# Kernel tuning notes

Measured on AMD Instinct MI355X. Metric: run time of the kernel, lower is better.

## Reference

```python
import jax, jax.numpy as jnp
import numpy as np

N = 50000
E = 800000
NEG_SLOPE = 0.2


def gatv2_layer(x, src, dst, Wl, Wr, att, bias, heads, ch):
    # x: [N, Fin]; Wl/Wr: [Fin, heads*ch]; att: [heads, ch]; bias: [heads*ch]
    xl = (x @ Wl).reshape(N, heads, ch)  # source transform
    xr = (x @ Wr).reshape(N, heads, ch)  # target transform
    e = xl[src] + xr[dst]                              # [E, H, C]
    s = jnp.einsum('ehc,hc->eh', jax.nn.leaky_relu(e, NEG_SLOPE), att)  # [E, H]
    # scatter-softmax over incoming edges of each target node
    smax = jax.ops.segment_max(s, dst, num_segments=N)  # [N, H]
    ex = jnp.exp(s - smax[dst])
    denom = jax.ops.segment_sum(ex, dst, num_segments=N)
    alpha = ex / denom[dst]                             # [E, H]
    out = jax.ops.segment_sum(xl[src] * alpha[..., None], dst, num_segments=N)  # [N, H, C]
    return out.reshape(N, heads * ch) + bias


def setup_inputs() -> dict:
    key = jax.random.key(0)
    ks = jax.random.split(key, 12)
    x = jax.random.normal(ks[0], (N, 128), dtype=jnp.float32)
    edge_index = jax.random.randint(ks[1], (2, E), 0, N, dtype=jnp.int64)
    edge_attr = jax.random.normal(ks[2], (E, 16), dtype=jnp.float32)
    s1 = 1.0 / np.sqrt(128.0)
    # layer 1: 128 -> 64, heads=2 (concat -> 128)
    Wl1 = jax.random.normal(ks[3], (128, 128), dtype=jnp.float32) * s1
    Wr1 = jax.random.normal(ks[4], (128, 128), dtype=jnp.float32) * s1
    att1 = jax.random.normal(ks[5], (2, 64), dtype=jnp.float32) * 0.1
    b1 = jnp.zeros((128,), dtype=jnp.float32)
    # layer 2: 128 -> 128, heads=1
    Wl2 = jax.random.normal(ks[6], (128, 128), dtype=jnp.float32) * s1
    Wr2 = jax.random.normal(ks[7], (128, 128), dtype=jnp.float32) * s1
    att2 = jax.random.normal(ks[8], (1, 128), dtype=jnp.float32) * 0.1
    b2 = jnp.zeros((128,), dtype=jnp.float32)
    return {"x": x, "edge_index": edge_index, "edge_attr": edge_attr,
            "Wl1": Wl1, "Wr1": Wr1, "att1": att1, "b1": b1,
            "Wl2": Wl2, "Wr2": Wr2, "att2": att2, "b2": b2}


def reference(x, edge_index, edge_attr, Wl1, Wr1, att1, b1, Wl2, Wr2, att2, b2):
    # using_edge_attr=False default path: edge_attr ignored.
    # GATv2Conv default add_self_loops=True
    loops = jnp.arange(N, dtype=edge_index.dtype)
    src = jnp.concatenate([edge_index[0], loops])
    dst = jnp.concatenate([edge_index[1], loops])
    h = gatv2_layer(x, src, dst, Wl1, Wr1, att1, b1, heads=2, ch=64)
    out = gatv2_layer(h, src, dst, Wl2, Wr2, att2, b2, heads=1, ch=128)
    return out
```

## Files before the change

kernel.cpp:

```cpp
#include <hip/hip_runtime.h>

#define NEG_SLOPE 0.2f
#define NPB 256
#define CHUNK 4096
#define BCAP 5120

typedef _Float16 f16x8 __attribute__((ext_vector_type(8)));
typedef _Float16 f16x4 __attribute__((ext_vector_type(4)));
typedef _Float16 f16x2 __attribute__((ext_vector_type(2)));
typedef float    f32x4 __attribute__((ext_vector_type(4)));
typedef float    f32x8 __attribute__((ext_vector_type(8)));

#if defined(__has_builtin)
#if __has_builtin(__builtin_amdgcn_fdot2)
#define HAVE_FDOT2 1
#endif
#endif

__device__ __forceinline__ f32x8 cvt8(f16x8 v) {
    return __builtin_convertvector(v, f32x8);
}

template <int CTRL>
__device__ __forceinline__ float dpp_add(float v) {
    int o = __builtin_amdgcn_update_dpp(0, __builtin_bit_cast(int, v),
                                        CTRL, 0xF, 0xF, true);
    return v + __builtin_bit_cast(float, o);
}

__global__ __launch_bounds__(256) void prep_kernel(
    const float* __restrict__ W0, const float* __restrict__ W1,
    const float* __restrict__ W2, const float* __restrict__ W3,
    _Float16* __restrict__ wt,
    const float* __restrict__ x, _Float16* __restrict__ xh,
    _Float16* __restrict__ xlo, int total, int* __restrict__ gcursor)
{
    int t = threadIdx.x;
    if (blockIdx.x < 256) {
        if (blockIdx.x == 0) gcursor[t] = t * BCAP;
        int idx = blockIdx.x * 256 + t;
        int m = idx >> 14;
        int k = (idx >> 7) & 127;
        int n = idx & 127;
        const float* W = (m == 0) ? W0 : (m == 1) ? W1 : (m == 2) ? W2 : W3;
        wt[m * 16384 + n * 128 + k] = (_Float16)W[k * 128 + n];
    } else {
        int i = (blockIdx.x - 256) * 256 + t;
        if (i * 2 < total) {
            float2 f = *(const float2*)(x + (size_t)i * 2);
            _Float16 h0 = (_Float16)f.x, h1 = (_Float16)f.y;
            _Float16 l0 = (_Float16)(f.x - (float)h0), l1 = (_Float16)(f.y - (float)h1);
            *(f16x2*)(xh  + (size_t)i * 2) = (f16x2){h0, h1};
            *(f16x2*)(xlo + (size_t)i * 2) = (f16x2){l0, l1};
        }
    }
}

__global__ __launch_bounds__(256) void gemm_f16_kernel(
    const _Float16* __restrict__ Ahi, const _Float16* __restrict__ Alo,
    const _Float16* __restrict__ Wt0, const _Float16* __restrict__ Wt1,
    _Float16* __restrict__ Cl, _Float16* __restrict__ Cr, int N)
{
    __shared__ _Float16 ldsW[128 * 136];

    const int tid = threadIdx.x;
    const int wave = tid >> 6;
    const int lane = tid & 63;
    const int mrow = lane & 15;
    const int quad = lane >> 4;
    const int rbase = blockIdx.x * 128 + wave * 32;
    const int sn = tid >> 1, shf = tid & 1;

    float4 stg[8];
    {
        const float4* gp = (const float4*)(Wt0 + sn * 128 + shf * 64);
#pragma unroll
        for (int j = 0; j < 8; j++) stg[j] = gp[j];
    }

    f16x8 ah[2][4], al[2][4];
#pragma unroll
    for (int rt = 0; rt < 2; rt++) {
        int r = rbase + rt * 16 + mrow;
        if (r > N - 1) r = N - 1;
        const _Float16* pa = Ahi + (size_t)r * 128 + quad * 8;
        const _Float16* pl = Alo + (size_t)r * 128 + quad * 8;
#pragma unroll
        for (int s = 0; s < 4; s++) {
            ah[rt][s] = *(const f16x8*)(pa + s * 32);
            al[rt][s] = *(const f16x8*)(pl + s * 32);
        }
    }

    {
        float4* d = (float4*)&ldsW[sn * 136 + shf * 64];
#pragma unroll
        for (int j = 0; j < 8; j++) d[j] = stg[j];
    }
    __syncthreads();

    float4 stg1[8];
    {
        const float4* gp = (const float4*)(Wt1 + sn * 128 + shf * 64);
#pragma unroll
        for (int j = 0; j < 8; j++) stg1[j] = gp[j];
    }

    auto compute_store = [&](_Float16* __restrict__ C) {
        f32x4 acc[2][8];
#pragma unroll
        for (int rt = 0; rt < 2; rt++)
#pragma unroll
            for (int c = 0; c < 8; c++) acc[rt][c] = (f32x4){0.f, 0.f, 0.f, 0.f};

#pragma unroll
        for (int s = 0; s < 4; s++) {
#pragma unroll
            for (int c = 0; c < 8; c++) {
                f16x8 bw = *(const f16x8*)&ldsW[(c * 16 + mrow) * 136 + s * 32 + quad * 8];
                acc[0][c] = __builtin_amdgcn_mfma_f32_16x16x32_f16(ah[0][s], bw, acc[0][c], 0, 0, 0);
                acc[0][c] = __builtin_amdgcn_mfma_f32_16x16x32_f16(al[0][s], bw, acc[0][c], 0, 0, 0);
                acc[1][c] = __builtin_amdgcn_mfma_f32_16x16x32_f16(ah[1][s], bw, acc[1][c], 0, 0, 0);
                acc[1][c] = __builtin_amdgcn_mfma_f32_16x16x32_f16(al[1][s], bw, acc[1][c], 0, 0, 0);
            }
        }

#pragma unroll
        for (int rt = 0; rt < 2; rt++)
#pragma unroll
            for (int i = 0; i < 4; i++) {
                int r = rbase + rt * 16 + quad * 4 + i;
                if (r < N) {
                    _Float16* cr = C + (size_t)r * 128 + mrow;
#pragma unroll
                    for (int c = 0; c < 8; c++) cr[c * 16] = (_Float16)acc[rt][c][i];
                }
            }
    };

    compute_store(Cl);

    __syncthreads();
    {
        float4* d = (float4*)&ldsW[sn * 136 + shf * 64];
#pragma unroll
        for (int j = 0; j < 8; j++) d[j] = stg1[j];
    }
    __syncthreads();

    compute_store(Cr);
}

__global__ __launch_bounds__(256) void bucketA_kernel(
    const int* __restrict__ ei, int* __restrict__ gcursor,
    int2* __restrict__ staging, int E)
{
    __shared__ int bh[256];
    __shared__ int bbase[256];
    int t = threadIdx.x;
    bh[t] = 0;
    __syncthreads();
    int base = blockIdx.x * CHUNK;
    int srcv[16], dstv[16], rb[16];
#pragma unroll
    for (int j = 0; j < 16; j++) {
        int e = base + t + j * 256;
        if (e < E) {
            int d = ei[E + e];
            srcv[j] = ei[e];
            dstv[j] = d;
            int bk = d >> 8;
            int r = atomicAdd(&bh[bk], 1);
            rb[j] = (r << 8) | bk;
        } else rb[j] = -1;
    }
    __syncthreads();
    if (bh[t]) bbase[t] = atomicAdd(&gcursor[t], bh[t]);
    __syncthreads();
#pragma unroll
    for (int j = 0; j < 16; j++) {
        if (rb[j] >= 0) {
            int bk = rb[j] & 255, r = rb[j] >> 8;
            staging[bbase[bk] + r] = make_int2(srcv[j], dstv[j]);
        }
    }
}

__global__ __launch_bounds__(256) void passB_kernel(
    const int2* __restrict__ staging, const int* __restrict__ gcursor,
    int* __restrict__ start, int* __restrict__ deg,
    int* __restrict__ sorted_src, int N)
{
    __shared__ int lhist[256], lscan[256], lcur[256];
    int b = blockIdx.x, t = threadIdx.x;
    int r0 = b * BCAP;
    int r1 = gcursor[b];
    lhist[t] = 0;
    __syncthreads();
    for (int i = r0 + t; i < r1; i += 256) atomicAdd(&lhist[staging[i].y & 255], 1);
    __syncthreads();
    int v = lhist[t];
    lscan[t] = v;
    __syncthreads();
    for (int off = 1; off < 256; off <<= 1) {
        int u = (t >= off) ? lscan[t - off] : 0;
        __syncthreads();
        lscan[t] += u;
        __syncthreads();
    }
    int excl = lscan[t] - v;
    int node = b * NPB + t;
    if (node < N) { start[node] = r0 + excl; deg[node] = v; }
    lcur[t] = excl;
    __syncthreads();
    for (int i = r0 + t; i < r1; i += 256) {
        int2 p = staging[i];
        int rank = atomicAdd(&lcur[p.y & 255], 1);
        sorted_src[r0 + rank] = p.x;
    }
}

template <int H, bool BFOUT>
__global__ __launch_bounds__(256) void gat_fused_kernel(
    const _Float16* __restrict__ xl, const _Float16* __restrict__ xr,
    const float* __restrict__ att, const float* __restrict__ bias,
    const int* __restrict__ start, const int* __restrict__ deg,
    const int* __restrict__ sorted_src,
    float* __restrict__ outf, _Float16* __restrict__ oh,
    _Float16* __restrict__ ol, int N)
{
    int node = blockIdx.x * 4 + (threadIdx.x >> 6);
    if (node >= N) return;
    const int lane = threadIdx.x & 63;
    const int g  = lane >> 4;
    const int hl = lane & 15;
    const _Float16 NS = (_Float16)NEG_SLOPE;
    const float L2E = 1.44269504f;

    const f16x8 b4 = *(const f16x8*)(xr + (size_t)node * 128 + hl * 8);
    float4 at0 = *(const float4*)(att + hl * 8);
    float4 at1 = *(const float4*)(att + hl * 8 + 4);
#if defined(HAVE_FDOT2)
    f16x2 av0 = {(_Float16)(at0.x * L2E), (_Float16)(at0.y * L2E)};
    f16x2 av1 = {(_Float16)(at0.z * L2E), (_Float16)(at0.w * L2E)};
    f16x2 av2 = {(_Float16)(at1.x * L2E), (_Float16)(at1.y * L2E)};
    f16x2 av3 = {(_Float16)(at1.z * L2E), (_Float16)(at1.w * L2E)};
#else
    f32x8 avf = {at0.x * L2E, at0.y * L2E, at0.z * L2E, at0.w * L2E,
                 at1.x * L2E, at1.y * L2E, at1.z * L2E, at1.w * L2E};
#endif

    auto score = [&](f16x8 a_) -> float {
        f16x8 t = a_ + b4;
        f16x8 u = __builtin_elementwise_max(t, t * NS);
#if defined(HAVE_FDOT2)
        f16x2 u0 = __builtin_shufflevector(u, u, 0, 1);
        f16x2 u1 = __builtin_shufflevector(u, u, 2, 3);
        f16x2 u2 = __builtin_shufflevector(u, u, 4, 5);
        f16x2 u3 = __builtin_shufflevector(u, u, 6, 7);
        return __builtin_amdgcn_fdot2(u0, av0,
               __builtin_amdgcn_fdot2(u1, av1,
               __builtin_amdgcn_fdot2(u2, av2,
               __builtin_amdgcn_fdot2(u3, av3, 0.f, false), false), false), false);
#else
        f32x8 uf = cvt8(u);
        float p = 0.f;
#pragma unroll
        for (int i = 0; i < 8; i++) p += uf[i] * avf[i];
        return p;
#endif
    };

    auto red = [&](float p) -> float {
        p = dpp_add<0xB1>(p);
        p = dpp_add<0x4E>(p);
        p = dpp_add<0x141>(p);
        if (H == 1) p = dpp_add<0x140>(p);
        return p;
    };

    f32x8 acc = {0.f, 0.f, 0.f, 0.f, 0.f, 0.f, 0.f, 0.f};
    float den = 0.f;

    const int s0 = start[node];
    const int M  = deg[node] + 1;
    const int Kfull = M >> 2;
    const int K     = (M + 3) >> 2;

#define GBODY(B) {                                                          \
        int srcv[B]; f16x8 a[B]; float p[B];                                \
        _Pragma("unroll")                                                   \
        for (int j = 0; j < B; j++) {                                       \
            int iv = 4 * (k + j) + g;                                       \
            int ld = sorted_src[s0 + ((iv > 0) ? iv - 1 : 0)];              \
            srcv[j] = (iv == 0) ? node : ld;                                \
        }                                                                   \
        _Pragma("unroll")                                                   \
        for (int j = 0; j < B; j++)                                         \
            a[j] = *(const f16x8*)(xl + (size_t)srcv[j] * 128 + hl * 8);    \
        _Pragma("unroll")                                                   \
        for (int j = 0; j < B; j++) p[j] = score(a[j]);                     \
        _Pragma("unroll")                                                   \
        for (int j = 0; j < B; j++) p[j] = red(p[j]);                       \
        _Pragma("unroll")                                                   \
        for (int j = 0; j < B; j++) {                                       \
            float e = exp2f(p[j]);                                          \
            den += e;                                                       \
            acc = acc + cvt8(a[j]) * e;                                     \
        }                                                                   \
    }

    int k = 0;
    for (; k + 4 <= Kfull; k += 4) GBODY(4)
    if (k + 2 <= Kfull) { GBODY(2) k += 2; }
    if (k < Kfull)      { GBODY(1) k += 1; }
    if (k < K) {
        int iv = 4 * k + g;
        bool valid = iv < M;
        int ld = sorted_src[s0 + ((iv > 0) ? iv - 1 : 0)];
        int src = (iv == 0) ? node : (valid ? ld : node);
        f16x8 a = *(const f16x8*)(xl + (size_t)src * 128 + hl * 8);
        float p = red(score(a));
        float e = valid ? exp2f(p) : 0.f;
        den += e;
        acc = acc + cvt8(a) * e;
    }
#undef GBODY

    den += __shfl_xor(den, 16, 64);
    den += __shfl_xor(den, 32, 64);
#pragma unroll
    for (int i = 0; i < 8; i++) {
        acc[i] += __shfl_xor(acc[i], 16, 64);
        acc[i] += __shfl_xor(acc[i], 32, 64);
    }

    float inv = 1.0f / den;
    float4 bi0 = *(const float4*)(bias + hl * 8);
    float4 bi1 = *(const float4*)(bias + hl * 8 + 4);
    float o[8];
    o[0] = acc[0] * inv + bi0.x;  o[1] = acc[1] * inv + bi0.y;
    o[2] = acc[2] * inv + bi0.z;  o[3] = acc[3] * inv + bi0.w;
    o[4] = acc[4] * inv + bi1.x;  o[5] = acc[5] * inv + bi1.y;
    o[6] = acc[6] * inv + bi1.z;  o[7] = acc[7] * inv + bi1.w;

    if (lane < 16) {
        if (BFOUT) {
            f16x8 hv, lv;
#pragma unroll
            for (int i = 0; i < 8; i++) {
                _Float16 h = (_Float16)o[i];
                hv[i] = h;
                lv[i] = (_Float16)(o[i] - (float)h);
            }
            *(f16x8*)(oh + (size_t)node * 128 + hl * 8) = hv;
            *(f16x8*)(ol + (size_t)node * 128 + hl * 8) = lv;
        } else {
            *(float4*)(outf + (size_t)node * 128 + hl * 8) =
                make_float4(o[0], o[1], o[2], o[3]);
            *(float4*)(outf + (size_t)node * 128 + hl * 8 + 4) =
                make_float4(o[4], o[5], o[6], o[7]);
        }
    }
}

extern "C" void kernel_launch(void* const* d_in, const int* in_sizes, int n_in,
                              void* d_out, int out_size, void* d_ws, size_t ws_size,
                              hipStream_t stream)
{
    const float* x    = (const float*)d_in[0];
    const int*   ei   = (const int*)d_in[1];
    const float* Wl1  = (const float*)d_in[3];
    const float* Wr1  = (const float*)d_in[4];
    const float* att1 = (const float*)d_in[5];
    const float* b1   = (const float*)d_in[6];
    const float* Wl2  = (const float*)d_in[7];
    const float* Wr2  = (const float*)d_in[8];
    const float* att2 = (const float*)d_in[9];
    const float* b2   = (const float*)d_in[10];
    float* out = (float*)d_out;

    const int N  = in_sizes[0] / 128;
    const int E  = in_sizes[1] / 2;
    const int NB = (N + NPB - 1) / NPB;

    const size_t nf = (size_t)N * 128;
    _Float16* xlf  = (_Float16*)d_ws;
    _Float16* xrf  = xlf + nf;
    _Float16* ah   = xrf + nf;
    _Float16* al   = ah + nf;
    _Float16* wt   = al + nf;
    int* gcursor   = (int*)(wt + 4 * 16384);
    int* start     = gcursor + 256;
    int* deg       = start + N;
    size_t stgoff  = ((size_t)(deg + N) + 7) & ~(size_t)7;
    int2* staging  = (int2*)stgoff;
    int* sorted_src = (int*)(staging + (size_t)NB * BCAP);

    const int grid_chunk = (E + CHUNK - 1) / CHUNK;
    const int node_grid  = (N + 3) / 4;
    const int gemm_gx    = (N + 127) / 128;
    const int split_grid = (int)((nf / 2 + 255) / 256);

    prep_kernel<<<256 + split_grid, 256, 0, stream>>>(
        Wl1, Wr1, Wl2, Wr2, wt, x, ah, al, (int)nf, gcursor);

    bucketA_kernel<<<grid_chunk, 256, 0, stream>>>(ei, gcursor, staging, E);
    passB_kernel<<<NB, 256, 0, stream>>>(staging, gcursor, start, deg,
                                         sorted_src, N);

    gemm_f16_kernel<<<gemm_gx, 256, 0, stream>>>(
        ah, al, wt + 0 * 16384, wt + 1 * 16384, xlf, xrf, N);
    gat_fused_kernel<2, true><<<node_grid, 256, 0, stream>>>(
        xlf, xrf, att1, b1, start, deg, sorted_src, nullptr, ah, al, N);

    gemm_f16_kernel<<<gemm_gx, 256, 0, stream>>>(
        ah, al, wt + 2 * 16384, wt + 3 * 16384, xlf, xrf, N);
    gat_fused_kernel<1, false><<<node_grid, 256, 0, stream>>>(
        xlf, xrf, att2, b2, start, deg, sorted_src, out, nullptr, nullptr, N);
}
```

Measured before the change: 286.5 us.

## Split GEMM over grid y and process two nodes per wave with software-pipelined gathers

The GEMM kernel now handles one weight matrix per block, using blockIdx.y to choose between Wl and Wr. This doubles the grid and drops the second LDS reload and its barriers. The aggregation kernel now has each wave process two target nodes at once and prefetches the next pair of gather groups while scoring the current ones. The aim is more memory-level parallelism to hide gather latency. In exchange, the A rows are loaded twice in the GEMM, and wave work is padded to the larger degree of the two nodes, so some iterations are wasted.

```diff
diff --git a/kernel.cpp b/kernel.cpp
--- a/kernel.cpp
+++ b/kernel.cpp
@@ -61,6 +61,9 @@
     const _Float16* __restrict__ Wt0, const _Float16* __restrict__ Wt1,
     _Float16* __restrict__ Cl, _Float16* __restrict__ Cr, int N)
 {
+    const _Float16* Wt = blockIdx.y ? Wt1 : Wt0;
+    _Float16* C = blockIdx.y ? Cr : Cl;
+
     __shared__ _Float16 ldsW[128 * 136];
 
     const int tid = threadIdx.x;
@@ -69,13 +72,13 @@
     const int mrow = lane & 15;
     const int quad = lane >> 4;
     const int rbase = blockIdx.x * 128 + wave * 32;
+
     const int sn = tid >> 1, shf = tid & 1;
-
     float4 stg[8];
     {
-        const float4* gp = (const float4*)(Wt0 + sn * 128 + shf * 64);
-#pragma unroll
-        for (int j = 0; j < 8; j++) stg[j] = gp[j];
+        const float4* g = (const float4*)(Wt + sn * 128 + shf * 64);
+#pragma unroll
+        for (int j = 0; j < 8; j++) stg[j] = g[j];
     }
 
     f16x8 ah[2][4], al[2][4];
@@ -97,58 +100,38 @@
 #pragma unroll
         for (int j = 0; j < 8; j++) d[j] = stg[j];
     }
-    __syncthreads();
-
-    float4 stg1[8];
-    {
-        const float4* gp = (const float4*)(Wt1 + sn * 128 + shf * 64);
-#pragma unroll
-        for (int j = 0; j < 8; j++) stg1[j] = gp[j];
-    }
-
-    auto compute_store = [&](_Float16* __restrict__ C) {
-        f32x4 acc[2][8];
-#pragma unroll
-        for (int rt = 0; rt < 2; rt++)
-#pragma unroll
-            for (int c = 0; c < 8; c++) acc[rt][c] = (f32x4){0.f, 0.f, 0.f, 0.f};
-
-#pragma unroll
-        for (int s = 0; s < 4; s++) {
-#pragma unroll
-            for (int c = 0; c < 8; c++) {
-                f16x8 bw = *(const f16x8*)&ldsW[(c * 16 + mrow) * 136 + s * 32 + quad * 8];
-                acc[0][c] = __builtin_amdgcn_mfma_f32_16x16x32_f16(ah[0][s], bw, acc[0][c], 0, 0, 0);
-                acc[0][c] = __builtin_amdgcn_mfma_f32_16x16x32_f16(al[0][s], bw, acc[0][c], 0, 0, 0);
-                acc[1][c] = __builtin_amdgcn_mfma_f32_16x16x32_f16(ah[1][s], bw, acc[1][c], 0, 0, 0);
-                acc[1][c] = __builtin_amdgcn_mfma_f32_16x16x32_f16(al[1][s], bw, acc[1][c], 0, 0, 0);
+
+    f32x4 acc[2][8];
+#pragma unroll
+    for (int rt = 0; rt < 2; rt++)
+#pragma unroll
+        for (int c = 0; c < 8; c++) acc[rt][c] = (f32x4){0.f, 0.f, 0.f, 0.f};
+
+    __syncthreads();
+
+#pragma unroll
+    for (int s = 0; s < 4; s++) {
+#pragma unroll
+        for (int c = 0; c < 8; c++) {
+            f16x8 bw = *(const f16x8*)&ldsW[(c * 16 + mrow) * 136 + s * 32 + quad * 8];
+            acc[0][c] = __builtin_amdgcn_mfma_f32_16x16x32_f16(ah[0][s], bw, acc[0][c], 0, 0, 0);
+            acc[0][c] = __builtin_amdgcn_mfma_f32_16x16x32_f16(al[0][s], bw, acc[0][c], 0, 0, 0);
+            acc[1][c] = __builtin_amdgcn_mfma_f32_16x16x32_f16(ah[1][s], bw, acc[1][c], 0, 0, 0);
+            acc[1][c] = __builtin_amdgcn_mfma_f32_16x16x32_f16(al[1][s], bw, acc[1][c], 0, 0, 0);
+        }
+    }
+
+#pragma unroll
+    for (int rt = 0; rt < 2; rt++)
+#pragma unroll
+        for (int i = 0; i < 4; i++) {
+            int r = rbase + rt * 16 + quad * 4 + i;
+            if (r < N) {
+                _Float16* cr = C + (size_t)r * 128 + mrow;
+#pragma unroll
+                for (int c = 0; c < 8; c++) cr[c * 16] = (_Float16)acc[rt][c][i];
             }
         }
-
-#pragma unroll
-        for (int rt = 0; rt < 2; rt++)
-#pragma unroll
-            for (int i = 0; i < 4; i++) {
-                int r = rbase + rt * 16 + quad * 4 + i;
-                if (r < N) {
-                    _Float16* cr = C + (size_t)r * 128 + mrow;
-#pragma unroll
-                    for (int c = 0; c < 8; c++) cr[c * 16] = (_Float16)acc[rt][c][i];
-                }
-            }
-    };
-
-    compute_store(Cl);
-
-    __syncthreads();
-    {
-        float4* d = (float4*)&ldsW[sn * 136 + shf * 64];
-#pragma unroll
-        for (int j = 0; j < 8; j++) d[j] = stg1[j];
-    }
-    __syncthreads();
-
-    compute_store(Cr);
 }
 
 __global__ __launch_bounds__(256) void bucketA_kernel(
@@ -229,15 +212,19 @@
     float* __restrict__ outf, _Float16* __restrict__ oh,
     _Float16* __restrict__ ol, int N)
 {
-    int node = blockIdx.x * 4 + (threadIdx.x >> 6);
-    if (node >= N) return;
+    const int wid = threadIdx.x >> 6;
+    const int n0 = blockIdx.x * 8 + wid * 2;
+    if (n0 >= N) return;
+    const bool has1 = (n0 + 1) < N;
+    const int n1 = has1 ? n0 + 1 : n0;
     const int lane = threadIdx.x & 63;
     const int g  = lane >> 4;
     const int hl = lane & 15;
     const _Float16 NS = (_Float16)NEG_SLOPE;
     const float L2E = 1.44269504f;
 
-    const f16x8 b4 = *(const f16x8*)(xr + (size_t)node * 128 + hl * 8);
+    const f16x8 b40 = *(const f16x8*)(xr + (size_t)n0 * 128 + hl * 8);
+    const f16x8 b41 = *(const f16x8*)(xr + (size_t)n1 * 128 + hl * 8);
     float4 at0 = *(const float4*)(att + hl * 8);
     float4 at1 = *(const float4*)(att + hl * 8 + 4);
 #if defined(HAVE_FDOT2)
@@ -250,8 +237,8 @@
                  at1.x * L2E, at1.y * L2E, at1.z * L2E, at1.w * L2E};
 #endif
 
-    auto score = [&](f16x8 a_) -> float {
-        f16x8 t = a_ + b4;
+    auto score = [&](f16x8 a_, f16x8 b4_) -> float {
+        f16x8 t = a_ + b4_;
         f16x8 u = __builtin_elementwise_max(t, t * NS);
 #if defined(HAVE_FDOT2)
         f16x2 u0 = __builtin_shufflevector(u, u, 0, 1);
@@ -279,72 +266,82 @@
         return p;
     };
 
-    f32x8 acc = {0.f, 0.f, 0.f, 0.f, 0.f, 0.f, 0.f, 0.f};
-    float den = 0.f;
-
-    const int s0 = start[node];
-    const int M  = deg[node] + 1;
-    const int Kfull = M >> 2;
-    const int K     = (M + 3) >> 2;
-
-#define GBODY(B) {                                                          \
-        int srcv[B]; f16x8 a[B]; float p[B];                                \
-        _Pragma("unroll")                                                   \
-        for (int j = 0; j < B; j++) {                                       \
-            int iv = 4 * (k + j) + g;                                       \
-            int ld = sorted_src[s0 + ((iv > 0) ? iv - 1 : 0)];              \
-            srcv[j] = (iv == 0) ? node : ld;                                \
-        }                                                                   \
-        _Pragma("unroll")                                                   \
-        for (int j = 0; j < B; j++)                                         \
-            a[j] = *(const f16x8*)(xl + (size_t)srcv[j] * 128 + hl * 8);    \
-        _Pragma("unroll")                                                   \
-        for (int j = 0; j < B; j++) p[j] = score(a[j]);                     \
-        _Pragma("unroll")                                                   \
-        for (int j = 0; j < B; j++) p[j] = red(p[j]);                       \
-        _Pragma("unroll")                                                   \
-        for (int j = 0; j < B; j++) {                                       \
-            float e = exp2f(p[j]);                                          \
-            den += e;                                                       \
-            acc = acc + cvt8(a[j]) * e;                                     \
-        }                                                                   \
-    }
-
-    int k = 0;
-    for (; k + 4 <= Kfull; k += 4) GBODY(4)
-    if (k + 2 <= Kfull) { GBODY(2) k += 2; }
-    if (k < Kfull)      { GBODY(1) k += 1; }
-    if (k < K) {
-        int iv = 4 * k + g;
-        bool valid = iv < M;
-        int ld = sorted_src[s0 + ((iv > 0) ? iv - 1 : 0)];
-        int src = (iv == 0) ? node : (valid ? ld : node);
-        f16x8 a = *(const f16x8*)(xl + (size_t)src * 128 + hl * 8);
-        float p = red(score(a));
-        float e = valid ? exp2f(p) : 0.f;
-        den += e;
-        acc = acc + cvt8(a) * e;
-    }
-#undef GBODY
-
-    den += __shfl_xor(den, 16, 64);
-    den += __shfl_xor(den, 32, 64);
+    const int s00 = start[n0];
+    const int M0  = deg[n0] + 1;
+    const int s01 = start[n1];
+    const int M1  = deg[n1] + 1;
+    const int Mmax = (M0 > M1) ? M0 : M1;
+    const int K   = (Mmax + 3) >> 2;
+    const int KK  = (K + 1) & ~1;
+
+    auto ldone = [&](int kk, int s0_, int M_, int nn) -> f16x8 {
+        int iv = 4 * kk + g;
+        int pos = s0_ + ((iv > 0) ? iv - 1 : 0);
+        int ld = sorted_src[pos];
+        int src = (iv == 0 || iv >= M_) ? nn : ld;
+        return *(const f16x8*)(xl + (size_t)src * 128 + hl * 8);
+    };
+
+    f32x8 acc0 = {0.f, 0.f, 0.f, 0.f, 0.f, 0.f, 0.f, 0.f};
+    f32x8 acc1 = {0.f, 0.f, 0.f, 0.f, 0.f, 0.f, 0.f, 0.f};
+    float den0 = 0.f, den1 = 0.f;
+
+    auto cone = [&](int kk, f16x8 a, f16x8 b4_, int M_, float& den_, f32x8& acc_) {
+        float p = red(score(a, b4_));
+        float e = (4 * kk + g < M_) ? exp2f(p) : 0.f;
+        den_ += e;
+#pragma unroll
+        for (int i = 0; i < 8; i++)
+            acc_[i] = fmaf((float)a[i], e, acc_[i]);
+    };
+
+    f16x8 c00 = ldone(0, s00, M0, n0);
+    f16x8 c01 = ldone(0, s01, M1, n1);
+    f16x8 c10 = ldone(1, s00, M0, n0);
+    f16x8 c11 = ldone(1, s01, M1, n1);
+    int k = 2;
+    for (; k < KK; k += 2) {
+        f16x8 d00 = ldone(k,     s00, M0, n0);
+        f16x8 d01 = ldone(k,     s01, M1, n1);
+        f16x8 d10 = ldone(k + 1, s00, M0, n0);
+        f16x8 d11 = ldone(k + 1, s01, M1, n1);
+        cone(k - 2, c00, b40, M0, den0, acc0);
+        cone(k - 2, c01, b41, M1, den1, acc1);
+        cone(k - 1, c10, b40, M0, den0, acc0);
+        cone(k - 1, c11, b41, M1, den1, acc1);
+        c00 = d00; c01 = d01; c10 = d10; c11 = d11;
+    }
+    cone(KK - 2, c00, b40, M0, den0, acc0);
+    cone(KK - 2, c01, b41, M1, den1, acc1);
+    cone(KK - 1, c10, b40, M0, den0, acc0);
+    cone(KK - 1, c11, b41, M1, den1, acc1);
+
+    den0 += __shfl_xor(den0, 16, 64);
+    den0 += __shfl_xor(den0, 32, 64);
+    den1 += __shfl_xor(den1, 16, 64);
+    den1 += __shfl_xor(den1, 32, 64);
 #pragma unroll
     for (int i = 0; i < 8; i++) {
-        acc[i] += __shfl_xor(acc[i], 16, 64);
-        acc[i] += __shfl_xor(acc[i], 32, 64);
-    }
-
-    float inv = 1.0f / den;
-    float4 bi0 = *(const float4*)(bias + hl * 8);
-    float4 bi1 = *(const float4*)(bias + hl * 8 + 4);
-    float o[8];
-    o[0] = acc[0] * inv + bi0.x;  o[1] = acc[1] * inv + bi0.y;
-    o[2] = acc[2] * inv + bi0.z;  o[3] = acc[3] * inv + bi0.w;
-    o[4] = acc[4] * inv + bi1.x;  o[5] = acc[5] * inv + bi1.y;
-    o[6] = acc[6] * inv + bi1.z;  o[7] = acc[7] * inv + bi1.w;
-
-    if (lane < 16) {
+        acc0[i] += __shfl_xor(acc0[i], 16, 64);
+        acc0[i] += __shfl_xor(acc0[i], 32, 64);
+        acc1[i] += __shfl_xor(acc1[i], 16, 64);
+        acc1[i] += __shfl_xor(acc1[i], 32, 64);
+    }
+
+    const int which = lane >> 4;
+    if (which == 0 || (which == 1 && has1)) {
+        float inv = 1.0f / (which == 0 ? den0 : den1);
+        int nodeo = (which == 0) ? n0 : n1;
+        float4 bi0 = *(const float4*)(bias + hl * 8);
+        float4 bi1 = *(const float4*)(bias + hl * 8 + 4);
+        float o[8];
+#pragma unroll
+        for (int i = 0; i < 8; i++) {
+            float a = (which == 0) ? acc0[i] : acc1[i];
+            float b = (i < 4) ? ((i == 0) ? bi0.x : (i == 1) ? bi0.y : (i == 2) ? bi0.z : bi0.w)
+                              : ((i == 4) ? bi1.x : (i == 5) ? bi1.y : (i == 6) ? bi1.z : bi1.w);
+            o[i] = a * inv + b;
+        }
         if (BFOUT) {
             f16x8 hv, lv;
 #pragma unroll
@@ -353,12 +350,12 @@
                 hv[i] = h;
                 lv[i] = (_Float16)(o[i] - (float)h);
             }
-            *(f16x8*)(oh + (size_t)node * 128 + hl * 8) = hv;
-            *(f16x8*)(ol + (size_t)node * 128 + hl * 8) = lv;
+            *(f16x8*)(oh + (size_t)nodeo * 128 + hl * 8) = hv;
+            *(f16x8*)(ol + (size_t)nodeo * 128 + hl * 8) = lv;
         } else {
-            *(float4*)(outf + (size_t)node * 128 + hl * 8) =
+            *(float4*)(outf + (size_t)nodeo * 128 + hl * 8) =
                 make_float4(o[0], o[1], o[2], o[3]);
-            *(float4*)(outf + (size_t)node * 128 + hl * 8 + 4) =
+            *(float4*)(outf + (size_t)nodeo * 128 + hl * 8 + 4) =
                 make_float4(o[4], o[5], o[6], o[7]);
         }
     }
@@ -398,7 +395,7 @@
     int* sorted_src = (int*)(staging + (size_t)NB * BCAP);
 
     const int grid_chunk = (E + CHUNK - 1) / CHUNK;
-    const int node_grid  = (N + 3) / 4;
+    const int node_grid  = (N + 7) / 8;
     const int gemm_gx    = (N + 127) / 128;
     const int split_grid = (int)((nf / 2 + 255) / 256);
 
@@ -409,12 +406,12 @@
     passB_kernel<<<NB, 256, 0, stream>>>(staging, gcursor, start, deg,
                                          sorted_src, N);
 
-    gemm_f16_kernel<<<gemm_gx, 256, 0, stream>>>(
+    gemm_f16_kernel<<<dim3(gemm_gx, 2), 256, 0, stream>>>(
         ah, al, wt + 0 * 16384, wt + 1 * 16384, xlf, xrf, N);
     gat_fused_kernel<2, true><<<node_grid, 256, 0, stream>>>(
         xlf, xrf, att1, b1, start, deg, sorted_src, nullptr, ah, al, N);
 
-    gemm_f16_kernel<<<gemm_gx, 256, 0, stream>>>(
+    gemm_f16_kernel<<<dim3(gemm_gx, 2), 256, 0, stream>>>(
         ah, al, wt + 2 * 16384, wt + 3 * 16384, xlf, xrf, N);
     gat_fused_kernel<1, false><<<node_grid, 256, 0, stream>>>(
         xlf, xrf, att2, b2, start, deg, sorted_src, out, nullptr, nullptr, N);
```

New measurement: 276.8 us. 1.03x faster.
